# Performance work log

Measured on AMD Instinct MI355X. Metric: run time of the kernel, lower is better.

## Reference

```python
import jax, jax.numpy as jnp
import numpy as np

D_HIDDEN = 1024
N_HEAD = 16
D_HEAD = D_HIDDEN // N_HEAD  # 64
B, F = 4, 2048


def setup_inputs() -> dict:
    key = jax.random.key(0)
    ks = jax.random.split(key, 10)
    std = 0.02
    inp = {
        "q": jax.random.normal(ks[0], (B, F, D_HIDDEN), jnp.float32),
        "k": jax.random.normal(ks[1], (B, F, D_HIDDEN), jnp.float32),
        "v": jax.random.normal(ks[2], (B, F, D_HIDDEN), jnp.float32),
        # additive mask: 1 = masked position (scaled by -1e9 inside); all-zero = no masking
        "attention_mask": jnp.zeros((B, F, F), jnp.float32),
        # Dense layer params (Keras Dense: y = x @ W + b)
        "qw_w": jax.random.truncated_normal(ks[3], -2, 2, (D_HIDDEN, D_HIDDEN), jnp.float32) * std,
        "qw_b": jnp.zeros((D_HIDDEN,), jnp.float32),
        "kw_w": jax.random.truncated_normal(ks[4], -2, 2, (D_HIDDEN, D_HIDDEN), jnp.float32) * std,
        "kw_b": jnp.zeros((D_HIDDEN,), jnp.float32),
        "vw_w": jax.random.truncated_normal(ks[5], -2, 2, (D_HIDDEN, D_HIDDEN), jnp.float32) * std,
        "vw_b": jnp.zeros((D_HIDDEN,), jnp.float32),
        # output projection kernel (n_head, d_head, d_hidden)
        "out_kernel": jax.random.truncated_normal(ks[6], -2, 2, (N_HEAD, D_HEAD, D_HIDDEN), jnp.float32) * std,
    }
    return inp


def reference(q, k, v, attention_mask, qw_w, qw_b, kw_w, kw_b, vw_w, vw_b, out_kernel):
    b, f, _ = q.shape
    # linear projections
    qh = q @ qw_w + qw_b
    kh = k @ kw_w + kw_b
    vh = v @ vw_w + vw_b
    # split heads: [B, F, H, D] -> [B, H, F, D]
    def split(x):
        return x.reshape(b, -1, N_HEAD, D_HEAD).transpose(0, 2, 1, 3)
    qh, kh, vh = split(qh), split(kh), split(vh)
    # scaled dot-product attention with additive mask (1 -> -1e9)
    scores = jnp.einsum('BNFD,BNfD->BNFf', qh, kh) / jnp.sqrt(jnp.asarray(D_HEAD, qh.dtype))
    scores = scores + attention_mask[:, None, :, :] * jnp.asarray(-1e9, scores.dtype)
    probs = jax.nn.softmax(scores, axis=-1)
    out = jnp.einsum('BNFf,BNfD->BNFD', probs, vh)
    out = out.transpose(0, 2, 1, 3)  # BNFD -> BFND
    return jnp.einsum('BFND,NDM->BFM', out, out_kernel)
```

## Files before the change

### kernel.cpp

```cpp
#include <hip/hip_runtime.h>


typedef unsigned short u16;
typedef __attribute__((ext_vector_type(8))) short short8;
typedef __attribute__((ext_vector_type(4))) float f32x4;
typedef __attribute__((ext_vector_type(16))) float f32x16;

#define SC2 0.18033688011112042f
#define MSC -1.4426950408889634e9f
#define THR 8.0f

__device__ __forceinline__ u16 f2bf(float x) {
  unsigned int u = __float_as_uint(x);
  u += 0x7FFFu + ((u >> 16) & 1u);
  return (u16)(u >> 16);
}

__device__ __forceinline__ void gload16(const void* g, void* l) {
  __builtin_amdgcn_global_load_lds(
      (const __attribute__((address_space(1))) void*)g,
      (__attribute__((address_space(3))) void*)l, 16, 0, 0);
}

__device__ __forceinline__ uint4 pack8(const u16* t) {
  uint4 o;
  o.x = (unsigned)t[0] | ((unsigned)t[1] << 16);
  o.y = (unsigned)t[2] | ((unsigned)t[3] << 16);
  o.z = (unsigned)t[4] | ((unsigned)t[5] << 16);
  o.w = (unsigned)t[6] | ((unsigned)t[7] << 16);
  return o;
}

__device__ __forceinline__ unsigned cvtpk(float lo, float hi) {
  unsigned r;
  asm("v_cvt_pk_bf16_f32 %0, %1, %2" : "=v"(r) : "v"(lo), "v"(hi));
  return r;
}

__global__ __launch_bounds__(256) void cvt3(const float* __restrict__ q,
                                            const float* __restrict__ k,
                                            const float* __restrict__ v,
                                            u16* __restrict__ dq,
                                            u16* __restrict__ dk,
                                            u16* __restrict__ dv) {
  const float* s;
  u16* d;
  switch (blockIdx.y) {
    case 0: s = q; d = dq; break;
    case 1: s = k; d = dk; break;
    default: s = v; d = dv; break;
  }
  int i = blockIdx.x * 256 + threadIdx.x;
  const float4* sp = (const float4*)s;
  float4 a = sp[2 * i], b = sp[2 * i + 1];
  uint4 o;
  o.x = (unsigned)f2bf(a.x) | ((unsigned)f2bf(a.y) << 16);
  o.y = (unsigned)f2bf(a.z) | ((unsigned)f2bf(a.w) << 16);
  o.z = (unsigned)f2bf(b.x) | ((unsigned)f2bf(b.y) << 16);
  o.w = (unsigned)f2bf(b.z) | ((unsigned)f2bf(b.w) << 16);
  ((uint4*)d)[i] = o;
}

__global__ __launch_bounds__(256) void masksum(const float* __restrict__ mask,
                                               unsigned char* __restrict__ msum) {
  int t = blockIdx.x * 256 + threadIdx.x;
  int row = t & 2047;
  int kt = (t >> 11) & 31;
  int b = t >> 16;
  const float4* p =
      (const float4*)(mask + ((size_t)(b * 2048 + row)) * 2048 + kt * 64);
  unsigned acc = 0;
#pragma unroll
  for (int i = 0; i < 16; i++) {
    float4 f = p[i];
    acc |= __float_as_uint(f.x) | __float_as_uint(f.y) |
           __float_as_uint(f.z) | __float_as_uint(f.w);
  }
  msum[t] = acc ? 1 : 0;
}

__global__ __launch_bounds__(256) void wtrans(
    const float* __restrict__ w0, const float* __restrict__ w1,
    const float* __restrict__ w2, const float* __restrict__ w3,
    u16* __restrict__ o0, u16* __restrict__ o1,
    u16* __restrict__ o2, u16* __restrict__ o3) {
  const float* W; u16* O;
  switch (blockIdx.z) {
    case 0: W = w0; O = o0; break;
    case 1: W = w1; O = o1; break;
    case 2: W = w2; O = o2; break;
    default: W = w3; O = o3; break;
  }
  __shared__ u16 T[64][72];
  const int t = threadIdx.x, r = t >> 2, seg = t & 3;
  const int k0 = blockIdx.y * 64, n0 = blockIdx.x * 64;
  const float* src = W + (size_t)(k0 + r) * 1024 + n0 + seg * 16;
#pragma unroll
  for (int jj = 0; jj < 4; jj++) {
    float4 f = ((const float4*)src)[jj];
    T[r][seg * 16 + jj * 4 + 0] = f2bf(f.x);
    T[r][seg * 16 + jj * 4 + 1] = f2bf(f.y);
    T[r][seg * 16 + jj * 4 + 2] = f2bf(f.z);
    T[r][seg * 16 + jj * 4 + 3] = f2bf(f.w);
  }
  __syncthreads();
  u16 tmp[16];
#pragma unroll
  for (int j = 0; j < 16; j++) tmp[j] = T[seg * 16 + j][r];
  u16* dst = O + (size_t)(n0 + r) * 1024 + k0 + seg * 16;
  ((uint4*)dst)[0] = pack8(tmp);
  ((uint4*)dst)[1] = pack8(tmp + 8);
}

__global__ __launch_bounds__(256) void gemm_proj3(
    const u16* __restrict__ Aq, const u16* __restrict__ Ak,
    const u16* __restrict__ Av, const u16* __restrict__ Wq,
    const u16* __restrict__ Wk, const u16* __restrict__ Wv,
    const float* __restrict__ bq, const float* __restrict__ bk,
    const float* __restrict__ bv, u16* __restrict__ oq,
    u16* __restrict__ ok, u16* __restrict__ ovT) {
  constexpr int K = 1024, N = 1024;
  __shared__ u16 sbuf[128 * 136];
  u16* lsA = sbuf;
  u16* lsB = sbuf + 128 * 32;
  const int z = blockIdx.z;
  const u16* A  = (z == 0) ? Aq : (z == 1) ? Ak : Av;
  const u16* Bt = (z == 0) ? Wq : (z == 1) ? Wk : Wv;
  const float* bias = (z == 0) ? bq : (z == 1) ? bk : bv;

  const int tid = threadIdx.x;
  const int w = tid >> 6, lane = tid & 63;
  const int l15 = lane & 15, lg = lane >> 4;
  const int m0 = blockIdx.y << 7, n0 = blockIdx.x << 7;
  const int wr = w >> 1, wc = w & 1;

  f32x4 acc[4][4];
#pragma unroll
  for (int i = 0; i < 4; i++)
#pragma unroll
    for (int j = 0; j < 4; j++) acc[i][j] = f32x4{0.f, 0.f, 0.f, 0.f};

  const u16* As = A + (size_t)(m0 + w * 32 + (lane >> 2)) * K + (lane & 3) * 8;
  const u16* Bs = Bt + (size_t)(n0 + w * 32 + (lane >> 2)) * K + (lane & 3) * 8;
  u16* lA = &lsA[(w * 32) * 32];
  u16* lB = &lsB[(w * 32) * 32];

  for (int k0 = 0; k0 < K; k0 += 32) {
    gload16(As + k0, lA);
    gload16(As + 16 * K + k0, lA + 16 * 32);
    gload16(Bs + k0, lB);
    gload16(Bs + 16 * K + k0, lB + 16 * 32);
    __syncthreads();
    short8 af[4], bfv[4];
#pragma unroll
    for (int mi = 0; mi < 4; mi++)
      af[mi] = *(const short8*)&lsA[(wr * 64 + mi * 16 + l15) * 32 + lg * 8];
#pragma unroll
    for (int nj = 0; nj < 4; nj++)
      bfv[nj] = *(const short8*)&lsB[(wc * 64 + nj * 16 + l15) * 32 + lg * 8];
#pragma unroll
    for (int mi = 0; mi < 4; mi++)
#pragma unroll
      for (int nj = 0; nj < 4; nj++)
        acc[mi][nj] = __builtin_amdgcn_mfma_f32_16x16x32_bf16(af[mi], bfv[nj],
                                                              acc[mi][nj], 0, 0, 0);
    __syncthreads();
  }

  const int crow = m0 + wr * 64 + lg * 4;
  const int ccol = n0 + wc * 64 + l15;
  if (z < 2) {
    u16* C = (z == 0) ? oq : ok;
    const float scl = (z == 0) ? SC2 : 1.0f;
#pragma unroll
    for (int nj = 0; nj < 4; nj++) {
      float bv = bias[ccol + nj * 16];
#pragma unroll
      for (int mi = 0; mi < 4; mi++)
#pragma unroll
        for (int r = 0; r < 4; r++)
          C[(size_t)(crow + mi * 16 + r) * N + ccol + nj * 16] =
              f2bf((acc[mi][nj][r] + bv) * scl);
    }
  } else {
    const int rl = wr * 64 + lg * 4;
    const int cl = wc * 64 + l15;
#pragma unroll
    for (int nj = 0; nj < 4; nj++) {
      float bv = bias[ccol + nj * 16];
#pragma unroll
      for (int mi = 0; mi < 4; mi++)
#pragma unroll
        for (int r = 0; r < 4; r++)
          sbuf[(rl + mi * 16 + r) * 136 + cl + nj * 16] =
              f2bf(acc[mi][nj][r] + bv);
    }
    __syncthreads();
    const int drow = tid >> 1, seg = tid & 1;
    const int b = m0 >> 11;
    const int f0 = (m0 & 2047) + seg * 64;
    u16* dst = ovT + (size_t)(b * 1024 + n0 + drow) * 2048 + f0;
#pragma unroll
    for (int c = 0; c < 8; c++) {
      u16 tmp[8];
#pragma unroll
      for (int j = 0; j < 8; j++)
        tmp[j] = sbuf[(seg * 64 + c * 8 + j) * 136 + drow];
      ((uint4*)dst)[c] = pack8(tmp);
    }
  }
}

__global__ __launch_bounds__(256) void gemm_out(
    const u16* __restrict__ A, const u16* __restrict__ Bt,
    float* __restrict__ C) {
  constexpr int K = 1024, N = 1024;
  __shared__ u16 lsA[128 * 32];
  __shared__ u16 lsB[128 * 32];
  const int tid = threadIdx.x;
  const int w = tid >> 6, lane = tid & 63;
  const int l15 = lane & 15, lg = lane >> 4;
  const int m0 = blockIdx.y << 7, n0 = blockIdx.x << 7;
  const int wr = w >> 1, wc = w & 1;

  f32x4 acc[4][4];
#pragma unroll
  for (int i = 0; i < 4; i++)
#pragma unroll
    for (int j = 0; j < 4; j++) acc[i][j] = f32x4{0.f, 0.f, 0.f, 0.f};

  const u16* As = A + (size_t)(m0 + w * 32 + (lane >> 2)) * K + (lane & 3) * 8;
  const u16* Bs = Bt + (size_t)(n0 + w * 32 + (lane >> 2)) * K + (lane & 3) * 8;
  u16* lA = &lsA[(w * 32) * 32];
  u16* lB = &lsB[(w * 32) * 32];

  for (int k0 = 0; k0 < K; k0 += 32) {
    gload16(As + k0, lA);
    gload16(As + 16 * K + k0, lA + 16 * 32);
    gload16(Bs + k0, lB);
    gload16(Bs + 16 * K + k0, lB + 16 * 32);
    __syncthreads();
    short8 af[4], bfv[4];
#pragma unroll
    for (int mi = 0; mi < 4; mi++)
      af[mi] = *(const short8*)&lsA[(wr * 64 + mi * 16 + l15) * 32 + lg * 8];
#pragma unroll
    for (int nj = 0; nj < 4; nj++)
      bfv[nj] = *(const short8*)&lsB[(wc * 64 + nj * 16 + l15) * 32 + lg * 8];
#pragma unroll
    for (int mi = 0; mi < 4; mi++)
#pragma unroll
      for (int nj = 0; nj < 4; nj++)
        acc[mi][nj] = __builtin_amdgcn_mfma_f32_16x16x32_bf16(af[mi], bfv[nj],
                                                              acc[mi][nj], 0, 0, 0);
    __syncthreads();
  }

  const int crow = m0 + wr * 64 + lg * 4;
  const int ccol = n0 + wc * 64 + l15;
#pragma unroll
  for (int nj = 0; nj < 4; nj++)
#pragma unroll
    for (int mi = 0; mi < 4; mi++)
#pragma unroll
      for (int r = 0; r < 4; r++)
        C[(size_t)(crow + mi * 16 + r) * N + ccol + nj * 16] = acc[mi][nj][r];
}

__global__ __launch_bounds__(256, 4) void attn_fwd(
    const u16* __restrict__ qh, const u16* __restrict__ kh,
    const u16* __restrict__ vhT, const float* __restrict__ mask,
    const unsigned char* __restrict__ msum, u16* __restrict__ aout) {
  __shared__ u16 Kls[2][64][72];
  __shared__ u16 Vls[2][64][72];

  const int tid = threadIdx.x;
  const int w = tid >> 6, lane = tid & 63;
  const int l31 = lane & 31, hi = lane >> 5;
  const int blk = ((blockIdx.x & 7) << 7) | (blockIdx.x >> 3);
  const int qt = blk & 15, bh = blk >> 4, h = bh & 15, b = bh >> 4;
  const int frow = qt * 128 + w * 32;
  const size_t qrow0 = (size_t)b * 2048 + frow;

  short8 qf[4];
#pragma unroll
  for (int ds = 0; ds < 4; ds++)
    qf[ds] = *(const short8*)&qh[(qrow0 + l31) * 1024 + h * 64 + ds * 16 + hi * 8];

  f32x16 oacc[2];
#pragma unroll
  for (int i = 0; i < 16; i++) { oacc[0][i] = 0.f; oacc[1][i] = 0.f; }
  float m_run = 0.f, l_run = 0.f;

  const int sr = tid >> 2, seg = tid & 3;
  const u16* Ksrc = kh + ((size_t)b * 2048 + sr) * 1024 + h * 64 + seg * 16;
  const u16* Vsrc = vhT + ((size_t)bh * 64 + sr) * 2048 + seg * 16;
  const unsigned char* msrow = msum + (size_t)b * 65536 + frow + l31;

  uint4 ka0, ka1, va0, va1;
  unsigned char mb, mbn;
  {
    const uint4* kp = (const uint4*)Ksrc;
    uint4 x0 = kp[0], x1 = kp[1];
    const uint4* vp = (const uint4*)Vsrc;
    uint4 y0 = vp[0], y1 = vp[1];
    *(uint4*)&Kls[0][sr][seg * 16] = x0;
    *(uint4*)&Kls[0][sr][seg * 16 + 8] = x1;
    *(uint4*)&Vls[0][sr][seg * 16] = y0;
    *(uint4*)&Vls[0][sr][seg * 16 + 8] = y1;
    kp = (const uint4*)(Ksrc + 64 * 1024);
    ka0 = kp[0]; ka1 = kp[1];
    vp = (const uint4*)(Vsrc + 64);
    va0 = vp[0]; va1 = vp[1];
    mb = msrow[0];
    mbn = msrow[2048];
  }
  __syncthreads();

  for (int kt = 0; kt < 32; kt++) {
    const int cur = kt & 1;
    const int k0 = kt * 64;
    const int mflag = __any((int)mb);
    mb = mbn;

    if (kt < 31) {
      *(uint4*)&Kls[cur ^ 1][sr][seg * 16] = ka0;
      *(uint4*)&Kls[cur ^ 1][sr][seg * 16 + 8] = ka1;
      *(uint4*)&Vls[cur ^ 1][sr][seg * 16] = va0;
      *(uint4*)&Vls[cur ^ 1][sr][seg * 16 + 8] = va1;
    }
    if (kt < 30) {
      const uint4* kp = (const uint4*)(Ksrc + (size_t)(kt + 2) * 64 * 1024);
      ka0 = kp[0]; ka1 = kp[1];
      const uint4* vp = (const uint4*)(Vsrc + (kt + 2) * 64);
      va0 = vp[0]; va1 = vp[1];
      mbn = msrow[(size_t)(kt + 2) * 2048];
    }

    f32x16 sacc[2];
#pragma unroll
    for (int i = 0; i < 16; i++) { sacc[0][i] = 0.f; sacc[1][i] = 0.f; }
#pragma unroll
    for (int kb = 0; kb < 2; kb++) {
      short8 kf[4];
#pragma unroll
      for (int ds = 0; ds < 4; ds++)
        kf[ds] = *(const short8*)&Kls[cur][kb * 32 + l31][ds * 16 + hi * 8];
      __builtin_amdgcn_s_setprio(1);
#pragma unroll
      for (int ds = 0; ds < 4; ds++)
        sacc[kb] = __builtin_amdgcn_mfma_f32_32x32x16_bf16(kf[ds], qf[ds],
                                                           sacc[kb], 0, 0, 0);
      __builtin_amdgcn_s_setprio(0);
    }

    if (mflag) {
      const size_t mrow = ((size_t)b * 2048 + frow + l31) * 2048 + (size_t)k0;
#pragma unroll
      for (int kb = 0; kb < 2; kb++)
#pragma unroll
        for (int r = 0; r < 16; r++) {
          float mv = mask[mrow + kb * 32 + (r & 3) + 8 * (r >> 2) + 4 * hi];
          sacc[kb][r] = fmaf(mv, MSC, sacc[kb][r]);
        }
      float mx[16];
#pragma unroll
      for (int r = 0; r < 16; r++) mx[r] = fmaxf(sacc[0][r], sacc[1][r]);
#pragma unroll
      for (int s = 8; s >= 1; s >>= 1)
#pragma unroll
        for (int r = 0; r < s; r++) mx[r] = fmaxf(mx[r], mx[r + s]);
      float tm = mx[0];
      tm = fmaxf(tm, __shfl_xor(tm, 32, 64));
      if (!__all(tm <= m_run + THR)) {
        float mnew = fmaxf(m_run, tm);
        float al = exp2f(m_run - mnew);
        m_run = mnew;
        l_run *= al;
#pragma unroll
        for (int r = 0; r < 16; r++) {
          float alr = __shfl(al, (r & 3) + 8 * (r >> 2) + 4 * hi, 64);
          oacc[0][r] *= alr;
          oacc[1][r] *= alr;
        }
      }
    }

    float rsp = 0.f, rsq = 0.f;
    unsigned pw[16];
    if (m_run == 0.f) {
#pragma unroll
      for (int kb = 0; kb < 2; kb++)
#pragma unroll
        for (int jp = 0; jp < 2; jp++) {
          float e[8];
#pragma unroll
          for (int t = 0; t < 8; t++)
            e[t] = exp2f(sacc[kb][8 * jp + t]);
          rsp += (e[0] + e[1]) + (e[2] + e[3]);
          rsq += (e[4] + e[5]) + (e[6] + e[7]);
          unsigned ye0 = cvtpk(e[0], e[1]);
          unsigned ye1 = cvtpk(e[2], e[3]);
          unsigned xo0 = cvtpk(e[4], e[5]);
          unsigned xo1 = cvtpk(e[6], e[7]);
          asm volatile("v_permlane32_swap_b32 %0, %1" : "+v"(ye0), "+v"(xo0));
          asm volatile("v_permlane32_swap_b32 %0, %1" : "+v"(ye1), "+v"(xo1));
          const int kk = kb * 2 + jp;
          pw[kk * 4 + 0] = ye0;
          pw[kk * 4 + 1] = ye1;
          pw[kk * 4 + 2] = xo0;
          pw[kk * 4 + 3] = xo1;
        }
    } else {
      const float mm = m_run;
#pragma unroll
      for (int kb = 0; kb < 2; kb++)
#pragma unroll
        for (int jp = 0; jp < 2; jp++) {
          float e[8];
#pragma unroll
          for (int t = 0; t < 8; t++)
            e[t] = exp2f(sacc[kb][8 * jp + t] - mm);
          rsp += (e[0] + e[1]) + (e[2] + e[3]);
          rsq += (e[4] + e[5]) + (e[6] + e[7]);
          unsigned ye0 = cvtpk(e[0], e[1]);
          unsigned ye1 = cvtpk(e[2], e[3]);
          unsigned xo0 = cvtpk(e[4], e[5]);
          unsigned xo1 = cvtpk(e[6], e[7]);
          asm volatile("v_permlane32_swap_b32 %0, %1" : "+v"(ye0), "+v"(xo0));
          asm volatile("v_permlane32_swap_b32 %0, %1" : "+v"(ye1), "+v"(xo1));
          const int kk = kb * 2 + jp;
          pw[kk * 4 + 0] = ye0;
          pw[kk * 4 + 1] = ye1;
          pw[kk * 4 + 2] = xo0;
          pw[kk * 4 + 3] = xo1;
        }
    }
    float rs = rsp + rsq;
    rs += __shfl_xor(rs, 32, 64);
    l_run += rs;

#pragma unroll
    for (int dn = 0; dn < 2; dn++) {
      short8 vf[4];
#pragma unroll
      for (int kk = 0; kk < 4; kk++)
        vf[kk] = *(const short8*)&Vls[cur][dn * 32 + l31][kk * 16 + hi * 8];
      __builtin_amdgcn_s_setprio(1);
#pragma unroll
      for (int kk = 0; kk < 4; kk++) {
        uint4 t4 = {pw[kk * 4 + 0], pw[kk * 4 + 1], pw[kk * 4 + 2], pw[kk * 4 + 3]};
        oacc[dn] = __builtin_amdgcn_mfma_f32_32x32x16_bf16(
            *(short8*)&t4, vf[kk], oacc[dn], 0, 0, 0);
      }
      __builtin_amdgcn_s_setprio(0);
    }

    __syncthreads();
  }

  float inv = 1.0f / l_run;
#pragma unroll
  for (int r = 0; r < 16; r++) {
    const int qr = (r & 3) + 8 * (r >> 2) + 4 * hi;
    float invr = __shfl(inv, qr, 64);
    aout[(qrow0 + qr) * 1024 + h * 64 + l31] = f2bf(oacc[0][r] * invr);
    aout[(qrow0 + qr) * 1024 + h * 64 + 32 + l31] = f2bf(oacc[1][r] * invr);
  }
}

extern "C" void kernel_launch(void* const* d_in, const int* in_sizes, int n_in,
                              void* d_out, int out_size, void* d_ws, size_t ws_size,
                              hipStream_t stream) {
  (void)in_sizes; (void)n_in; (void)out_size; (void)ws_size;
  const float* q    = (const float*)d_in[0];
  const float* k    = (const float*)d_in[1];
  const float* v    = (const float*)d_in[2];
  const float* mask = (const float*)d_in[3];
  const float* qw_w = (const float*)d_in[4];
  const float* qw_b = (const float*)d_in[5];
  const float* kw_w = (const float*)d_in[6];
  const float* kw_b = (const float*)d_in[7];
  const float* vw_w = (const float*)d_in[8];
  const float* vw_b = (const float*)d_in[9];
  const float* wo   = (const float*)d_in[10];

  u16* qbf = (u16*)d_ws;
  u16* kbf = qbf + 8192 * 1024;
  u16* vbf = kbf + 8192 * 1024;
  u16* vhT = vbf + 8192 * 1024;
  u16* qwT = vhT + 8192 * 1024;
  u16* kwT = qwT + 1024 * 1024;
  u16* vwT = kwT + 1024 * 1024;
  u16* woT = vwT + 1024 * 1024;
  u16* attn_o = kbf;
  unsigned char* msumb = (unsigned char*)(woT + 1024 * 1024);
  u16* qh = (u16*)d_out;
  u16* kh = qh + 8192 * 1024;

  cvt3<<<dim3(4096, 3), 256, 0, stream>>>(q, k, v, qbf, kbf, vbf);
  wtrans<<<dim3(16, 16, 4), 256, 0, stream>>>(qw_w, kw_w, vw_w, wo,
                                              qwT, kwT, vwT, woT);
  gemm_proj3<<<dim3(8, 64, 3), 256, 0, stream>>>(qbf, kbf, vbf, qwT, kwT, vwT,
                                                 qw_b, kw_b, vw_b, qh, kh, vhT);
  masksum<<<1024, 256, 0, stream>>>(mask, msumb);
  attn_fwd<<<1024, 256, 0, stream>>>(qh, kh, vhT, mask, msumb, attn_o);
  gemm_out<<<dim3(8, 64), 256, 0, stream>>>(attn_o, woT, (float*)d_out);
}
```

Measured before the change: 276.4 us.

## Load K/V fragments directly from global into registers, dropping LDS staging

The attention kernel no longer stages K and V tiles through double-buffered shared memory. Each wave now loads its MFMA fragments straight from global memory into registers and prefetches the next tile after each MFMA phase, which also removes the per-iteration block barrier. The launch bounds drop from 4 to 2 blocks per CU so the larger register footprint fits. The cost is that every wave in a block fetches the same K/V data separately, relying on L1/L2 instead of LDS sharing, and occupancy is lower.

New measurement: 393.5 us. 42.4% more time.

```diff
diff --git a/kernel.cpp b/kernel.cpp
--- a/kernel.cpp
+++ b/kernel.cpp
@@ -267,13 +267,10 @@
         C[(size_t)(crow + mi * 16 + r) * N + ccol + nj * 16] = acc[mi][nj][r];
 }
 
-__global__ __launch_bounds__(256, 4) void attn_fwd(
+__global__ __launch_bounds__(256, 2) void attn_fwd(
     const u16* __restrict__ qh, const u16* __restrict__ kh,
     const u16* __restrict__ vhT, const float* __restrict__ mask,
     const unsigned char* __restrict__ msum, u16* __restrict__ aout) {
-  __shared__ u16 Kls[2][64][72];
-  __shared__ u16 Vls[2][64][72];
-
   const int tid = threadIdx.x;
   const int w = tid >> 6, lane = tid & 63;
   const int l31 = lane & 31, hi = lane >> 5;
@@ -292,66 +289,53 @@
   for (int i = 0; i < 16; i++) { oacc[0][i] = 0.f; oacc[1][i] = 0.f; }
   float m_run = 0.f, l_run = 0.f;
 
-  const int sr = tid >> 2, seg = tid & 3;
-  const u16* Ksrc = kh + ((size_t)b * 2048 + sr) * 1024 + h * 64 + seg * 16;
-  const u16* Vsrc = vhT + ((size_t)bh * 64 + sr) * 2048 + seg * 16;
+  const u16* Kb = kh + ((size_t)b * 2048 + l31) * 1024 + h * 64 + hi * 8;
+  const u16* Vb = vhT + ((size_t)bh * 64 + l31) * 2048 + hi * 8;
   const unsigned char* msrow = msum + (size_t)b * 65536 + frow + l31;
 
-  uint4 ka0, ka1, va0, va1;
-  unsigned char mb, mbn;
-  {
-    const uint4* kp = (const uint4*)Ksrc;
-    uint4 x0 = kp[0], x1 = kp[1];
-    const uint4* vp = (const uint4*)Vsrc;
-    uint4 y0 = vp[0], y1 = vp[1];
-    *(uint4*)&Kls[0][sr][seg * 16] = x0;
-    *(uint4*)&Kls[0][sr][seg * 16 + 8] = x1;
-    *(uint4*)&Vls[0][sr][seg * 16] = y0;
-    *(uint4*)&Vls[0][sr][seg * 16 + 8] = y1;
-    kp = (const uint4*)(Ksrc + 64 * 1024);
-    ka0 = kp[0]; ka1 = kp[1];
-    vp = (const uint4*)(Vsrc + 64);
-    va0 = vp[0]; va1 = vp[1];
-    mb = msrow[0];
-    mbn = msrow[2048];
-  }
-  __syncthreads();
+  short8 kf[2][4], vf[2][4];
+#pragma unroll
+  for (int kb = 0; kb < 2; kb++)
+#pragma unroll
+    for (int ds = 0; ds < 4; ds++)
+      kf[kb][ds] = *(const short8*)&Kb[(size_t)(kb * 32) * 1024 + ds * 16];
+#pragma unroll
+  for (int dn = 0; dn < 2; dn++)
+#pragma unroll
+    for (int kk = 0; kk < 2; kk++) {
+      vf[dn][2 * kk] = *(const short8*)&Vb[(size_t)(dn * 32) * 2048 + kk * 32];
+      vf[dn][2 * kk + 1] =
+          *(const short8*)&Vb[(size_t)(dn * 32) * 2048 + kk * 32 + 16];
+    }
+  unsigned char mb = msrow[0];
+  unsigned char mbn = msrow[2048];
 
   for (int kt = 0; kt < 32; kt++) {
-    const int cur = kt & 1;
     const int k0 = kt * 64;
+    const int ktn = (kt < 31) ? kt + 1 : 31;
     const int mflag = __any((int)mb);
     mb = mbn;
-
-    if (kt < 31) {
-      *(uint4*)&Kls[cur ^ 1][sr][seg * 16] = ka0;
-      *(uint4*)&Kls[cur ^ 1][sr][seg * 16 + 8] = ka1;
-      *(uint4*)&Vls[cur ^ 1][sr][seg * 16] = va0;
-      *(uint4*)&Vls[cur ^ 1][sr][seg * 16 + 8] = va1;
-    }
-    if (kt < 30) {
-      const uint4* kp = (const uint4*)(Ksrc + (size_t)(kt + 2) * 64 * 1024);
-      ka0 = kp[0]; ka1 = kp[1];
-      const uint4* vp = (const uint4*)(Vsrc + (kt + 2) * 64);
-      va0 = vp[0]; va1 = vp[1];
-      mbn = msrow[(size_t)(kt + 2) * 2048];
-    }
+    mbn = msrow[(size_t)((kt + 2 < 32) ? kt + 2 : 31) * 2048];
 
     f32x16 sacc[2];
 #pragma unroll
     for (int i = 0; i < 16; i++) { sacc[0][i] = 0.f; sacc[1][i] = 0.f; }
-#pragma unroll
-    for (int kb = 0; kb < 2; kb++) {
-      short8 kf[4];
+    __builtin_amdgcn_s_setprio(1);
+#pragma unroll
+    for (int kb = 0; kb < 2; kb++)
 #pragma unroll
       for (int ds = 0; ds < 4; ds++)
-        kf[ds] = *(const short8*)&Kls[cur][kb * 32 + l31][ds * 16 + hi * 8];
-      __builtin_amdgcn_s_setprio(1);
-#pragma unroll
-      for (int ds = 0; ds < 4; ds++)
-        sacc[kb] = __builtin_amdgcn_mfma_f32_32x32x16_bf16(kf[ds], qf[ds],
+        sacc[kb] = __builtin_amdgcn_mfma_f32_32x32x16_bf16(kf[kb][ds], qf[ds],
                                                            sacc[kb], 0, 0, 0);
-      __builtin_amdgcn_s_setprio(0);
+    __builtin_amdgcn_s_setprio(0);
+
+    {
+      const u16* Kn = Kb + (size_t)ktn * 64 * 1024;
+#pragma unroll
+      for (int kb = 0; kb < 2; kb++)
+#pragma unroll
+        for (int ds = 0; ds < 4; ds++)
+          kf[kb][ds] = *(const short8*)&Kn[(size_t)(kb * 32) * 1024 + ds * 16];
     }
 
     if (mflag) {
@@ -440,23 +424,26 @@
     rs += __shfl_xor(rs, 32, 64);
     l_run += rs;
 
-#pragma unroll
-    for (int dn = 0; dn < 2; dn++) {
-      short8 vf[4];
-#pragma unroll
-      for (int kk = 0; kk < 4; kk++)
-        vf[kk] = *(const short8*)&Vls[cur][dn * 32 + l31][kk * 16 + hi * 8];
-      __builtin_amdgcn_s_setprio(1);
+    __builtin_amdgcn_s_setprio(1);
+#pragma unroll
+    for (int dn = 0; dn < 2; dn++)
 #pragma unroll
       for (int kk = 0; kk < 4; kk++) {
         uint4 t4 = {pw[kk * 4 + 0], pw[kk * 4 + 1], pw[kk * 4 + 2], pw[kk * 4 + 3]};
         oacc[dn] = __builtin_amdgcn_mfma_f32_32x32x16_bf16(
-            *(short8*)&t4, vf[kk], oacc[dn], 0, 0, 0);
+            *(short8*)&t4, vf[dn][kk], oacc[dn], 0, 0, 0);
       }
-      __builtin_amdgcn_s_setprio(0);
-    }
-
-    __syncthreads();
+    __builtin_amdgcn_s_setprio(0);
+
+    {
+      const u16* Vn = Vb + ktn * 64;
+#pragma unroll
+      for (int dn = 0; dn < 2; dn++)
+#pragma unroll
+        for (int kk = 0; kk < 4; kk++)
+          vf[dn][kk] =
+              *(const short8*)&Vn[(size_t)(dn * 32) * 2048 + kk * 16];
+    }
   }
 
   float inv = 1.0f / l_run;
```
